# Optimization experiments

Measured on AMD Instinct MI355X. Metric: run time of the kernel, lower is better.

The kernel has to match this reference:

```python
import jax, jax.numpy as jnp
import numpy as np

N, S, L, K, D = 8, 2048, 8, 1024, 1024


def setup_inputs() -> dict:
    key = jax.random.key(0)
    k1, k2 = jax.random.split(key)
    x = jax.random.randint(k1, (N, S, L), 0, K, dtype=jnp.int64)
    weight = jax.random.normal(k2, (L, K, D), dtype=jnp.float32)
    return {"x": x, "weight": weight}


def reference(x, weight):
    # Original: one_hot(x.transpose(1,-1), K) then einsum 'l k d, n l s k -> n s d'
    # which is exactly out[n,s,d] = sum_l weight[l, x[n,s,l], d].
    L_ = weight.shape[0]
    lvl = jnp.arange(L_)  # (L,)
    # Advanced indexing: weight[l, x[n,s,l]] -> (N, S, L, D), then sum over levels.
    gathered = weight[lvl[None, None, :], x]  # (N, S, L, D)
    return gathered.sum(axis=2)  # (N, S, D)
```

## Files before the change

### kernel.cpp

```cpp
#include <hip/hip_runtime.h>
#include <hip/hip_bf16.h>


#define NS      (8 * 2048)
#define LVL     8
#define KK      1024
#define DD      1024
#define NCH     8
#define DCH     (DD / NCH)
#define ROWSPB  32
#define THREADS 256

typedef float f32x4 __attribute__((ext_vector_type(4)));

__global__ __launch_bounds__(THREADS, 4) void multi_embedding_kernel(
    const int* __restrict__ x,
    const float* __restrict__ w,
    float* __restrict__ out)
{
    const int chunk = blockIdx.x & (NCH - 1);
    const int nsg   = blockIdx.x >> 3;
    const int tid   = threadIdx.x;
    const int ns0   = nsg * ROWSPB;

    __shared__ int sidx[ROWSPB * LVL];
    sidx[tid] = x[(size_t)ns0 * LVL + tid];
    __syncthreads();
    const int4* s4 = reinterpret_cast<const int4*>(sidx);

    const int lane = tid & 31;
    const int rg   = tid >> 5;
    const float* wl = w + (size_t)chunk * DCH + (size_t)lane * 4;

#pragma unroll
    for (int rr = 0; rr < 2; ++rr) {
        const int rowA = rg + (2 * rr + 0) * 8;
        const int rowB = rg + (2 * rr + 1) * 8;

        const int4 a0 = s4[rowA * 2], a1 = s4[rowA * 2 + 1];
        const int4 b0 = s4[rowB * 2], b1 = s4[rowB * 2 + 1];
        const int idxA[LVL] = { a0.x, a0.y, a0.z, a0.w, a1.x, a1.y, a1.z, a1.w };
        const int idxB[LVL] = { b0.x, b0.y, b0.z, b0.w, b1.x, b1.y, b1.z, b1.w };

        f32x4 accA = (f32x4)0.f;
        f32x4 accB = (f32x4)0.f;
#pragma unroll
        for (int l = 0; l < LVL; ++l) {
            const f32x4 vA = *reinterpret_cast<const f32x4*>(
                wl + ((size_t)((l << 10) + idxA[l]) << 10));
            const f32x4 vB = *reinterpret_cast<const f32x4*>(
                wl + ((size_t)((l << 10) + idxB[l]) << 10));
            accA += vA;
            accB += vB;
        }

        f32x4* oA = reinterpret_cast<f32x4*>(
            out + (size_t)(ns0 + rowA) * DD + (size_t)chunk * DCH) + lane;
        f32x4* oB = reinterpret_cast<f32x4*>(
            out + (size_t)(ns0 + rowB) * DD + (size_t)chunk * DCH) + lane;
        __builtin_nontemporal_store(accA, oA);
        __builtin_nontemporal_store(accB, oB);
    }
}

extern "C" void kernel_launch(void* const* d_in, const int* in_sizes, int n_in,
                              void* d_out, int out_size, void* d_ws, size_t ws_size,
                              hipStream_t stream) {
    const int*   x = (const int*)d_in[0];
    const float* w = (const float*)d_in[1];
    float*     out = (float*)d_out;

    multi_embedding_kernel<<<dim3((NS / ROWSPB) * NCH), dim3(THREADS), 0, stream>>>(x, w, out);
}
```

Before: 108.7 us.

## Convert weights to fp16 in workspace and gather/accumulate in half precision

Adds a pre-pass kernel that converts the fp32 weight table to fp16 in the workspace. The gather kernel then reads half8 vectors and accumulates in fp16 before widening to fp32 for output. The intent is to halve gather bytes, at the cost of an extra full-table read/write pass each call and reduced accumulation precision.

```diff
diff --git a/kernel.cpp b/kernel.cpp
--- a/kernel.cpp
+++ b/kernel.cpp
@@ -1,5 +1,6 @@
 #include <hip/hip_runtime.h>
 #include <hip/hip_bf16.h>
+#include <hip/hip_fp16.h>
 
 
 #define NS      (8 * 2048)
@@ -11,11 +12,22 @@
 #define ROWSPB  32
 #define THREADS 256
 
-typedef float f32x4 __attribute__((ext_vector_type(4)));
+typedef _Float16 half8 __attribute__((ext_vector_type(8)));
+typedef float    f32x4 __attribute__((ext_vector_type(4)));
+typedef float    f32x8 __attribute__((ext_vector_type(8)));
+
+__global__ __launch_bounds__(THREADS) void convert_w_kernel(
+    const float* __restrict__ w, _Float16* __restrict__ wh)
+{
+    const size_t i = ((size_t)blockIdx.x * THREADS + threadIdx.x) * 8;
+    const f32x8 v = *reinterpret_cast<const f32x8*>(w + i);
+    const half8 h = __builtin_convertvector(v, half8);
+    *reinterpret_cast<half8*>(wh + i) = h;
+}
 
 __global__ __launch_bounds__(THREADS, 4) void multi_embedding_kernel(
     const int* __restrict__ x,
-    const float* __restrict__ w,
+    const _Float16* __restrict__ wh,
     float* __restrict__ out)
 {
     const int chunk = blockIdx.x & (NCH - 1);
@@ -28,39 +40,45 @@
     __syncthreads();
     const int4* s4 = reinterpret_cast<const int4*>(sidx);
 
-    const int lane = tid & 31;
-    const int rg   = tid >> 5;
-    const float* wl = w + (size_t)chunk * DCH + (size_t)lane * 4;
+    const int lane = tid & 15;
+    const int rg   = tid >> 4;
+    const _Float16* wl = wh + (size_t)chunk * DCH + (size_t)lane * 8;
 
+    const int rowA = rg;
+    const int rowB = rg + 16;
+
+    const int4 a0 = s4[rowA * 2], a1 = s4[rowA * 2 + 1];
+    const int4 b0 = s4[rowB * 2], b1 = s4[rowB * 2 + 1];
+    const int idxA[LVL] = { a0.x, a0.y, a0.z, a0.w, a1.x, a1.y, a1.z, a1.w };
+    const int idxB[LVL] = { b0.x, b0.y, b0.z, b0.w, b1.x, b1.y, b1.z, b1.w };
+
+    half8 accA = *reinterpret_cast<const half8*>(
+        wl + ((size_t)idxA[0] << 10));
+    half8 accB = *reinterpret_cast<const half8*>(
+        wl + ((size_t)idxB[0] << 10));
 #pragma unroll
-    for (int rr = 0; rr < 2; ++rr) {
-        const int rowA = rg + (2 * rr + 0) * 8;
-        const int rowB = rg + (2 * rr + 1) * 8;
+    for (int l = 1; l < LVL; ++l) {
+        const half8 vA = *reinterpret_cast<const half8*>(
+            wl + ((size_t)((l << 10) + idxA[l]) << 10));
+        const half8 vB = *reinterpret_cast<const half8*>(
+            wl + ((size_t)((l << 10) + idxB[l]) << 10));
+        accA += vA;
+        accB += vB;
+    }
 
-        const int4 a0 = s4[rowA * 2], a1 = s4[rowA * 2 + 1];
-        const int4 b0 = s4[rowB * 2], b1 = s4[rowB * 2 + 1];
-        const int idxA[LVL] = { a0.x, a0.y, a0.z, a0.w, a1.x, a1.y, a1.z, a1.w };
-        const int idxB[LVL] = { b0.x, b0.y, b0.z, b0.w, b1.x, b1.y, b1.z, b1.w };
+    const f32x8 fA = __builtin_convertvector(accA, f32x8);
+    const f32x8 fB = __builtin_convertvector(accB, f32x8);
+    const f32x4 fA_lo = __builtin_shufflevector(fA, fA, 0, 1, 2, 3);
+    const f32x4 fA_hi = __builtin_shufflevector(fA, fA, 4, 5, 6, 7);
+    const f32x4 fB_lo = __builtin_shufflevector(fB, fB, 0, 1, 2, 3);
+    const f32x4 fB_hi = __builtin_shufflevector(fB, fB, 4, 5, 6, 7);
 
-        f32x4 accA = (f32x4)0.f;
-        f32x4 accB = (f32x4)0.f;
-#pragma unroll
-        for (int l = 0; l < LVL; ++l) {
-            const f32x4 vA = *reinterpret_cast<const f32x4*>(
-                wl + ((size_t)((l << 10) + idxA[l]) << 10));
-            const f32x4 vB = *reinterpret_cast<const f32x4*>(
-                wl + ((size_t)((l << 10) + idxB[l]) << 10));
-            accA += vA;
-            accB += vB;
-        }
-
-        f32x4* oA = reinterpret_cast<f32x4*>(
-            out + (size_t)(ns0 + rowA) * DD + (size_t)chunk * DCH) + lane;
-        f32x4* oB = reinterpret_cast<f32x4*>(
-            out + (size_t)(ns0 + rowB) * DD + (size_t)chunk * DCH) + lane;
-        __builtin_nontemporal_store(accA, oA);
-        __builtin_nontemporal_store(accB, oB);
-    }
+    float* oA = out + (size_t)(ns0 + rowA) * DD + (size_t)chunk * DCH + (size_t)lane * 8;
+    float* oB = out + (size_t)(ns0 + rowB) * DD + (size_t)chunk * DCH + (size_t)lane * 8;
+    __builtin_nontemporal_store(fA_lo, reinterpret_cast<f32x4*>(oA));
+    __builtin_nontemporal_store(fA_hi, reinterpret_cast<f32x4*>(oA) + 1);
+    __builtin_nontemporal_store(fB_lo, reinterpret_cast<f32x4*>(oB));
+    __builtin_nontemporal_store(fB_hi, reinterpret_cast<f32x4*>(oB) + 1);
 }
 
 extern "C" void kernel_launch(void* const* d_in, const int* in_sizes, int n_in,
@@ -69,6 +87,9 @@
     const int*   x = (const int*)d_in[0];
     const float* w = (const float*)d_in[1];
     float*     out = (float*)d_out;
+    _Float16*   wh = (_Float16*)d_ws;
 
-    multi_embedding_kernel<<<dim3((NS / ROWSPB) * NCH), dim3(THREADS), 0, stream>>>(x, w, out);
+    convert_w_kernel<<<dim3((LVL * KK * DD) / (THREADS * 8)), dim3(THREADS), 0, stream>>>(w, wh);
+
+    multi_embedding_kernel<<<dim3((NS / ROWSPB) * NCH), dim3(THREADS), 0, stream>>>(x, wh, out);
 }
```

Measured after the change: 108.6 us. No clear change (-0.1%).
